# Performance work log

Hardware: AMD Instinct MI355X
Metric: run time of the kernel (lower is better)

Reference implementation:

```python
import jax, jax.numpy as jnp
from jax import lax
import numpy as np

EMBED, HIDDEN, VOCAB = 512, 512, 10000
ATT, ENC = 512, 2048
B, NPIX, T = 128, 49, 30


def _lin(k, out_d, in_d):
    k1, k2 = jax.random.split(k)
    s = 1.0 / np.sqrt(in_d)
    return (jax.random.uniform(k1, (out_d, in_d), minval=-s, maxval=s),
            jax.random.uniform(k2, (out_d,), minval=-s, maxval=s))


def setup_inputs() -> dict:
    key = jax.random.key(0)
    ks = jax.random.split(key, 24)
    inp = {}
    inp['enc_image'] = jax.random.normal(ks[0], (B, NPIX, ENC))
    inp['global_features'] = jax.random.normal(ks[1], (B, ENC))
    inp['encoded_captions'] = jax.random.randint(ks[2], (B, T), 0, VOCAB)
    lens = jax.random.randint(ks[3], (B,), 1, T + 1).at[0].set(T)
    inp['caption_lengths'] = lens[:, None]
    # parameters
    inp['emb_W'] = jax.random.uniform(ks[4], (VOCAB, EMBED), minval=-0.1, maxval=0.1)
    inp['e2h_W'], inp['e2h_b'] = _lin(ks[5], HIDDEN, ENC)
    inp['gf_W'], inp['gf_b'] = _lin(ks[6], EMBED, ENC)
    inp['fc_W'] = jax.random.uniform(ks[7], (VOCAB, HIDDEN), minval=-0.1, maxval=0.1)
    inp['fc_b'] = jnp.zeros((VOCAB,))
    inp['lstm_Wih'], inp['lstm_bih'] = _lin(ks[8], 4 * HIDDEN, 2 * EMBED)
    inp['lstm_Whh'], inp['lstm_bhh'] = _lin(ks[9], 4 * HIDDEN, HIDDEN)
    inp['xg_W'], inp['xg_b'] = _lin(ks[10], HIDDEN, 2 * EMBED)
    inp['hg_W'], inp['hg_b'] = _lin(ks[11], HIDDEN, HIDDEN)
    inp['senaff_W'], inp['senaff_b'] = _lin(ks[12], HIDDEN, HIDDEN)
    inp['senatt_W'], inp['senatt_b'] = _lin(ks[13], ATT, HIDDEN)
    inp['haff_W'], inp['haff_b'] = _lin(ks[14], HIDDEN, HIDDEN)
    inp['hatt_W'], inp['hatt_b'] = _lin(ks[15], ATT, HIDDEN)
    inp['vatt_W'], inp['vatt_b'] = _lin(ks[16], ATT, HIDDEN)
    inp['alph_W'], inp['alph_b'] = _lin(ks[17], 1, ATT)
    inp['ctx_W'], inp['ctx_b'] = _lin(ks[18], HIDDEN, HIDDEN)
    return inp


def reference(enc_image, global_features, encoded_captions, caption_lengths,
              emb_W, e2h_W, e2h_b, gf_W, gf_b, fc_W, fc_b,
              lstm_Wih, lstm_bih, lstm_Whh, lstm_bhh,
              xg_W, xg_b, hg_W, hg_b,
              senaff_W, senaff_b, senatt_W, senatt_b,
              haff_W, haff_b, hatt_W, hatt_b,
              vatt_W, vatt_b, alph_W, alph_b, ctx_W, ctx_b):
    lengths = caption_lengths[:, 0]
    order = jnp.argsort(-lengths)                     # descending (stable)
    lengths = lengths[order]
    spatial = jax.nn.relu(jnp.einsum('bpe,he->bph', enc_image[order], e2h_W) + e2h_b)  # (B,NP,H)
    gimg = jax.nn.relu(global_features[order] @ gf_W.T + gf_b)                          # (B,E)
    embs = emb_W[encoded_captions[order]]                                               # (B,T,E)
    inputs = jnp.concatenate([embs, jnp.broadcast_to(gimg[:, None, :], embs.shape)], axis=-1)  # (B,T,2E)
    vattn = jnp.einsum('bph,ah->bpa', spatial, vatt_W) + vatt_b                         # (B,NP,A) hoisted
    h0 = jnp.zeros((spatial.shape[0], HIDDEN), spatial.dtype)
    c0 = h0

    def step(carry, xs):
        h, c = carry
        xt, mask = xs                                  # (B,2E), (B,) bool = row still active
        gates = xt @ lstm_Wih.T + lstm_bih + h @ lstm_Whh.T + lstm_bhh
        i, f, g, o = jnp.split(gates, 4, axis=-1)
        c_new = jax.nn.sigmoid(f) * c + jax.nn.sigmoid(i) * jnp.tanh(g)
        h_new = jax.nn.sigmoid(o) * jnp.tanh(c_new)
        st = jax.nn.sigmoid(xt @ xg_W.T + xg_b + h @ hg_W.T + hg_b) * jnp.tanh(c_new)  # sentinel
        sen_aff = jax.nn.relu(st @ senaff_W.T + senaff_b)    # (B,H)
        sen_att = sen_aff @ senatt_W.T + senatt_b            # (B,A)
        h_aff = jnp.tanh(h_new @ haff_W.T + haff_b)
        h_att = h_aff @ hatt_W.T + hatt_b
        att_feats = jnp.concatenate([vattn, sen_att[:, None, :]], axis=1)   # (B,NP+1,A)
        scores = jnp.tanh(att_feats + h_att[:, None, :]) @ alph_W[0] + alph_b[0]
        alpha = jax.nn.softmax(scores, axis=1)               # (B,NP+1)
        cat_feats = jnp.concatenate([spatial, sen_aff[:, None, :]], axis=1)
        context = jnp.einsum('bph,bp->bh', cat_feats, alpha)
        out_l = jnp.tanh((context + h_aff) @ ctx_W.T + ctx_b)
        pt = out_l @ fc_W.T + fc_b                           # dropout = identity (eval)
        m = mask[:, None]
        return (jnp.where(m, h_new, h), jnp.where(m, c_new, c)), jnp.where(m, pt, 0.0)

    masks = lengths[None, :] > jnp.arange(T)[:, None]        # (T,B) replicates shrinking batch_size_t
    _, preds = lax.scan(step, (h0, c0), (jnp.swapaxes(inputs, 0, 1), masks))
    return jnp.swapaxes(preds, 0, 1)                         # (B,T,VOCAB), sorted-by-length order
```

## Files before the change

kernel.cpp:

```cpp
#include <hip/hip_runtime.h>
#include <hip/hip_bf16.h>
#include <cstdint>
#include <cstddef>

#define DEVI __device__ __forceinline__

#define BB 128
#define TT 30
#define VOCAB 10000
#define ENCD 2048
#define NPIX 49
#define SLOT 65536

typedef __attribute__((ext_vector_type(8))) short bf16x8;
typedef __attribute__((ext_vector_type(4))) float f32x4;

DEVI float bf2f(unsigned short u){ union{float f; unsigned int i;} x; x.i=((unsigned)u)<<16; return x.f; }
DEVI unsigned short f2bf(float f){ union{float f; unsigned int i;} x; x.f=f; unsigned r=x.i + 0x7fffu + ((x.i>>16)&1u); return (unsigned short)(r>>16); }
DEVI float sigm(float x){ return 1.0f/(1.0f+expf(-x)); }
DEVI f32x4 mfma16(bf16x8 a, bf16x8 b, f32x4 c){ return __builtin_amdgcn_mfma_f32_16x16x32_bf16(a,b,c,0,0,0); }

DEVI void waitflags(int* flags, int thresh){
  __syncthreads();
  if(threadIdx.x < 64){
    for(;;){
      int v = (threadIdx.x<32) ? __hip_atomic_load(&flags[threadIdx.x], __ATOMIC_RELAXED, __HIP_MEMORY_SCOPE_AGENT)
                               : 0x7fffffff;
      if(__all(v >= thresh)) break;
      __builtin_amdgcn_s_sleep(1);
    }
    __builtin_amdgcn_fence(__ATOMIC_ACQUIRE, "agent");
  }
  __syncthreads();
}
DEVI void signal(int* flag, int val){
  __syncthreads();
  if(threadIdx.x==0) __hip_atomic_store(flag, val, __ATOMIC_RELEASE, __HIP_MEMORY_SCOPE_AGENT);
}

__global__ void k_sort(const int* __restrict__ lens, int* __restrict__ order, int* __restrict__ Bt){
  __shared__ int L[BB];
  int i = threadIdx.x;
  L[i] = lens[i];
  __syncthreads();
  int li = L[i]; int rank = 0;
  for(int j=0;j<BB;j++){ int lj=L[j]; rank += (lj>li) || (lj==li && j<i); }
  order[rank] = i;
  if(i<TT){ int c=0; for(int j=0;j<BB;j++) c += (L[j]>i); Bt[i]=c; }
}

struct WC13 { const float* src[13]; unsigned short* dst[13]; int n[13]; };
__global__ void k_wconv(WC13 wc){
  int stride = gridDim.x*blockDim.x;
  int tid0 = blockIdx.x*blockDim.x + threadIdx.x;
  for(int s=0;s<13;s++){
    const float4* src=(const float4*)wc.src[s];
    int n4 = wc.n[s]>>2;
    ushort4* dst=(ushort4*)wc.dst[s];
    for(int i=tid0;i<n4;i+=stride){
      float4 v=src[i];
      ushort4 o; o.x=f2bf(v.x); o.y=f2bf(v.y); o.z=f2bf(v.z); o.w=f2bf(v.w);
      dst[i]=o;
    }
  }
}

__global__ void k_xt(const int* __restrict__ caps, const int* __restrict__ order,
                     const float* __restrict__ embW, const unsigned short* __restrict__ gimg,
                     unsigned short* __restrict__ xt){
  int total=BB*TT*1024;
  for(int idx=blockIdx.x*blockDim.x+threadIdx.x; idx<total; idx+=gridDim.x*blockDim.x){
    int k=idx&1023; int bt=idx>>10; int t=bt%TT; int b=bt/TT;
    unsigned short v;
    if(k<512){ int tok=caps[order[b]*TT+t]; v=f2bf(embW[(size_t)tok*512+k]); }
    else v=gimg[b*512+(k-512)];
    xt[idx]=v;
  }
}

__global__ __launch_bounds__(256) void k_gemm_f32A2(
    const float* __restrict__ A, int lda, int rpb, const int* __restrict__ order,
    const unsigned short* __restrict__ W, const float* __restrict__ bias,
    unsigned short* __restrict__ out, int K)
{
  __shared__ unsigned short As[128][136];
  int tid=threadIdx.x, wave=tid>>6, lane=tid&63, l15=lane&15, l4=lane>>4;
  int mb = blockIdx.y*128;
  f32x4 acc[8][4];
  f32x4 z = {0.f,0.f,0.f,0.f};
  #pragma unroll
  for(int i=0;i<8;i++)
    #pragma unroll
    for(int j=0;j<4;j++) acc[i][j]=z;
  int cch=tid&15, r0=tid>>4;
  int nb = blockIdx.x*256 + wave*64;
  for(int kc=0;kc<K;kc+=128){
    __syncthreads();
    #pragma unroll
    for(int rp=0;rp<8;rp++){
      int r=r0+rp*16;
      int m=mb+r;
      int sb = order[m/rpb]*rpb + m%rpb;
      const float* p = A + (size_t)sb*lda + kc + cch*8;
      float4 v0=*(const float4*)p, v1=*(const float4*)(p+4);
      unsigned short* d=&As[r][cch*8];
      d[0]=f2bf(v0.x); d[1]=f2bf(v0.y); d[2]=f2bf(v0.z); d[3]=f2bf(v0.w);
      d[4]=f2bf(v1.x); d[5]=f2bf(v1.y); d[6]=f2bf(v1.z); d[7]=f2bf(v1.w);
    }
    __syncthreads();
    #pragma unroll
    for(int kk=0;kk<4;kk++){
      bf16x8 bfr[4];
      #pragma unroll
      for(int nt=0;nt<4;nt++)
        bfr[nt] = *(const bf16x8*)(W + (size_t)(nb+nt*16+l15)*K + kc + kk*32 + l4*8);
      #pragma unroll
      for(int mt=0;mt<8;mt++){
        bf16x8 af = *(const bf16x8*)&As[mt*16+l15][kk*32+l4*8];
        #pragma unroll
        for(int nt=0;nt<4;nt++) acc[mt][nt]=mfma16(af,bfr[nt],acc[mt][nt]);
      }
    }
  }
  #pragma unroll
  for(int nt=0;nt<4;nt++){
    int n = nb + nt*16 + l15;
    float bs = bias[n];
    #pragma unroll
    for(int mt=0;mt<8;mt++){
      #pragma unroll
      for(int j=0;j<4;j++){
        int row = mb + mt*16 + l4*4 + j;
        float v = acc[mt][nt][j]+bs; v = v>0.f ? v : 0.f;
        out[(size_t)row*512 + n] = f2bf(v);
      }
    }
  }
}

DEVI void dev_gemm512(unsigned short (*As)[136], const unsigned short* A, const unsigned short* W,
                      const float* bias, unsigned short* out, int act, int xtile, int mb){
  int tid=threadIdx.x, wave=tid>>6, lane=tid&63, l15=lane&15, l4=lane>>4;
  f32x4 acc[8];
  f32x4 z = {0.f,0.f,0.f,0.f};
  #pragma unroll
  for(int i=0;i<8;i++) acc[i]=z;
  int cch=tid&15, r0=tid>>4;
  int nrow = xtile*64 + wave*16 + l15;
  for(int kc=0;kc<512;kc+=128){
    __syncthreads();
    #pragma unroll
    for(int rp=0;rp<8;rp++){
      int r=r0+rp*16;
      *(uint4*)&As[r][cch*8] = *(const uint4*)(A + (size_t)(mb+r)*512 + kc + cch*8);
    }
    __syncthreads();
    #pragma unroll
    for(int kk=0;kk<4;kk++){
      bf16x8 bfr = *(const bf16x8*)(W + (size_t)nrow*512 + kc + kk*32 + l4*8);
      #pragma unroll
      for(int mt=0;mt<8;mt++){
        bf16x8 af = *(const bf16x8*)&As[mt*16+l15][kk*32+l4*8];
        acc[mt]=mfma16(af,bfr,acc[mt]);
      }
    }
  }
  float bs = bias ? bias[nrow] : 0.f;
  #pragma unroll
  for(int mt=0;mt<8;mt++){
    #pragma unroll
    for(int j=0;j<4;j++){
      int row = mb + mt*16 + l4*4 + j;
      float v = acc[mt][j]+bs;
      if(act==1) v = fmaxf(v,0.f);
      else if(act==2) v = tanhf(v);
      out[(size_t)row*512+nrow]=f2bf(v);
    }
  }
  __syncthreads();
}

struct PreD { const unsigned short* A; const unsigned short* W; const float* bias; unsigned short* out; };
struct PreD2 { PreD d[2]; };
__global__ __launch_bounds__(256) void k_pre(PreD2 dd){
  __shared__ unsigned short As[128][136];
  PreD g = dd.d[blockIdx.z];
  dev_gemm512(As, g.A, g.W, g.bias, g.out, 0, blockIdx.x, blockIdx.y*128);
}

struct PCtx {
  const unsigned short *xt, *w_ih, *w_hh, *w_xg, *w_hg;
  const unsigned short *w_saff, *w_satt, *w_haff, *w_hatt, *w_ctx, *w_fc;
  const unsigned short *vattn, *SC;
  const float *bih,*bhh,*bxg,*bhg, *sab,*stbias,*hab,*htb, *alW,*alb, *cxb, *fcb;
  const int *Bt;
  unsigned short *h_hist;
  unsigned short *stb;
  unsigned short *tbuf;
  float *dout;
  int *Lflag;
  int *Tflag;
};

DEVI void dev_lstm(unsigned short (*As)[136], const PCtx& p, int t, int jblk,
                   const unsigned short* hprev, unsigned short* hout, float creg[2][4]){
  int tid=threadIdx.x, wave=tid>>6, lane=tid&63, l15=lane&15, l4=lane>>4;
  int jb = jblk*16;
  f32x4 acc[2][5];
  f32x4 z = {0.f,0.f,0.f,0.f};
  #pragma unroll
  for(int m=0;m<2;m++)
    #pragma unroll
    for(int s=0;s<5;s++) acc[m][s]=z;
  int cch=tid&15, r0=tid>>4;
  for(int kc=0;kc<1536;kc+=128){
    __syncthreads();
    #pragma unroll
    for(int rp=0;rp<8;rp++){
      int r=r0+rp*16;
      int kg = kc + cch*8;
      const unsigned short* src;
      if(kg<1024) src = p.xt + (size_t)r*(TT*1024) + t*1024 + kg;
      else        src = hprev + (size_t)r*512 + (kg-1024);
      *(uint4*)&As[r][cch*8] = *(const uint4*)src;
    }
    __syncthreads();
    #pragma unroll
    for(int kk=0;kk<4;kk++){
      int kg = kc + kk*32 + l4*8;
      bf16x8 bfr[5];
      #pragma unroll
      for(int s=0;s<5;s++){
        int row = (s<4) ? (s*512 + jb + l15) : (jb + l15);
        const unsigned short* wp;
        if(s<4) wp = (kg<1024) ? (p.w_ih + (size_t)row*1024 + kg) : (p.w_hh + (size_t)row*512 + (kg-1024));
        else    wp = (kg<1024) ? (p.w_xg + (size_t)row*1024 + kg) : (p.w_hg + (size_t)row*512 + (kg-1024));
        bfr[s] = *(const bf16x8*)wp;
      }
      #pragma unroll
      for(int m=0;m<2;m++){
        int mt = wave*2+m;
        bf16x8 af = *(const bf16x8*)&As[mt*16+l15][kk*32+l4*8];
        #pragma unroll
        for(int s=0;s<5;s++) acc[m][s]=mfma16(af,bfr[s],acc[m][s]);
      }
    }
  }
  int bt = p.Bt[t];
  int j = jb + l15;
  float bi  = p.bih[j]      + p.bhh[j];
  float bff = p.bih[512+j]  + p.bhh[512+j];
  float bg  = p.bih[1024+j] + p.bhh[1024+j];
  float bo  = p.bih[1536+j] + p.bhh[1536+j];
  float bs  = p.bxg[j] + p.bhg[j];
  unsigned short* stt = p.stb + (size_t)t*SLOT;
  #pragma unroll
  for(int m=0;m<2;m++){
    int mt = wave*2+m;
    #pragma unroll
    for(int jj=0;jj<4;jj++){
      int b = mt*16 + l4*4 + jj;
      float iv = sigm(acc[m][0][jj]+bi);
      float fv = sigm(acc[m][1][jj]+bff);
      float gv = tanhf(acc[m][2][jj]+bg);
      float ov = sigm(acc[m][3][jj]+bo);
      float sv = sigm(acc[m][4][jj]+bs);
      float cn = fv*creg[m][jj] + iv*gv;
      float tc = tanhf(cn);
      size_t idx=(size_t)b*512+j;
      if(b<bt){ hout[idx]=f2bf(ov*tc); creg[m][jj]=cn; }
      else    { hout[idx]=hprev[idx]; }
      stt[idx]=f2bf(sv*tc);
    }
  }
}

DEVI void dev_attn(float* sS, float* sA, int b, const PCtx& p,
                   const unsigned short* satt, const unsigned short* hatt,
                   const unsigned short* scs, const unsigned short* sch,
                   unsigned short* outl){
  int tid=threadIdx.x; int gid=tid>>4, gl=tid&15;
  const unsigned short* ha = hatt + (size_t)b*512;
  #pragma unroll
  for(int rp=0;rp<4;rp++){
    int pp = rp*16 + gid;
    float s = 0.f;
    if(pp<50){
      const unsigned short* vp = (pp<NPIX) ? (p.vattn + ((size_t)b*NPIX + pp)*512)
                                           : (satt + (size_t)b*512);
      for(int k=gl*32;k<gl*32+32;k++) s += tanhf(bf2f(vp[k]) + bf2f(ha[k])) * p.alW[k];
    }
    #pragma unroll
    for(int off=8;off>=1;off>>=1) s += __shfl_xor(s, off);
    if(gl==0 && pp<50) sS[pp] = s + p.alb[0];
  }
  __syncthreads();
  if(tid==0){
    float m=-1e30f;
    for(int pp=0;pp<50;pp++) m = fmaxf(m, sS[pp]);
    float sum=0.f;
    for(int pp=0;pp<50;pp++){ float e=expf(sS[pp]-m); sA[pp]=e; sum+=e; }
    float inv=1.f/sum;
    for(int pp=0;pp<50;pp++) sA[pp]*=inv;
  }
  __syncthreads();
  float a49 = sA[49];
  for(int n=tid;n<512;n+=256){
    float acc = bf2f(sch[(size_t)b*512+n]) + a49*bf2f(scs[(size_t)b*512+n]) + p.cxb[n];
    const unsigned short* sp = p.SC + (size_t)b*NPIX*512 + n;
    for(int pp=0;pp<NPIX;pp++) acc += sA[pp]*bf2f(sp[(size_t)pp*512]);
    outl[(size_t)b*512+n] = f2bf(tanhf(acc));
  }
  __syncthreads();
}

DEVI void dev_fc(unsigned short (*As)[136], const PCtx& p, int t, int xtile,
                 const unsigned short* outl){
  int tid=threadIdx.x, wave=tid>>6, lane=tid&63, l15=lane&15, l4=lane>>4;
  int bt = p.Bt[t];
  f32x4 acc[8];
  f32x4 z = {0.f,0.f,0.f,0.f};
  #pragma unroll
  for(int i=0;i<8;i++) acc[i]=z;
  int cch=tid&15, r0=tid>>4;
  int nbase = xtile*64 + wave*16;
  int nr = nbase + l15; if(nr > VOCAB-1) nr = VOCAB-1;
  for(int kc=0;kc<512;kc+=128){
    __syncthreads();
    #pragma unroll
    for(int rp=0;rp<8;rp++){
      int r=r0+rp*16;
      *(uint4*)&As[r][cch*8] = *(const uint4*)(outl + (size_t)r*512 + kc + cch*8);
    }
    __syncthreads();
    #pragma unroll
    for(int kk=0;kk<4;kk++){
      bf16x8 bfr = *(const bf16x8*)(p.w_fc + (size_t)nr*512 + kc + kk*32 + l4*8);
      #pragma unroll
      for(int mt=0;mt<8;mt++){
        if(mt*16 < bt){
          bf16x8 af = *(const bf16x8*)&As[mt*16+l15][kk*32+l4*8];
          acc[mt]=mfma16(af,bfr,acc[mt]);
        }
      }
    }
  }
  int n = nbase + l15; bool nok = n < VOCAB;
  float bs = nok ? p.fcb[n] : 0.f;
  #pragma unroll
  for(int mt=0;mt<8;mt++){
    #pragma unroll
    for(int j=0;j<4;j++){
      int b = mt*16 + l4*4 + j;
      float v = (b<bt) ? (acc[mt][j]+bs) : 0.f;
      if(nok) p.dout[(size_t)b*(TT*VOCAB) + (size_t)t*VOCAB + n] = v;
    }
  }
  __syncthreads();
}

__global__ __launch_bounds__(256) void k_persist(PCtx p){
  __shared__ unsigned short As[128][136];
  __shared__ float sS[52];
  __shared__ float sA[52];
  int cb = blockIdx.x;
  if(cb < 32){
    float creg[2][4];
    #pragma unroll
    for(int m=0;m<2;m++)
      #pragma unroll
      for(int j=0;j<4;j++) creg[m][j]=0.f;
    for(int t=0;t<TT;t++){
      if(t>0) waitflags(p.Lflag, t);
      dev_lstm(As, p, t, cb, p.h_hist + (size_t)t*SLOT, p.h_hist + (size_t)(t+1)*SLOT, creg);
      signal(&p.Lflag[cb], t+1);
    }
  } else {
    int team = (cb-32)>>5, w = (cb-32)&31;
    unsigned short* S = p.tbuf + (size_t)team*7*SLOT;
    unsigned short *Saff=S, *Haff=S+SLOT, *Outl=S+2*SLOT, *Satt=S+3*SLOT,
                   *Hatt=S+4*SLOT, *Scs=S+5*SLOT, *Sch=S+6*SLOT;
    int* tf = p.Tflag + team*32;
    int it=0;
    for(int t=team; t<TT; t+=7, it++){
      waitflags(p.Lflag, t+1);
      if(w<8)       dev_gemm512(As, p.stb + (size_t)t*SLOT,        p.w_saff, p.sab, Saff, 1, w,   0);
      else if(w<16) dev_gemm512(As, p.h_hist + (size_t)(t+1)*SLOT, p.w_haff, p.hab, Haff, 2, w-8, 0);
      signal(&tf[w], it*3+1); waitflags(tf, it*3+1);
      if(w<8)       dev_gemm512(As, Saff, p.w_satt, p.stbias, Satt, 0, w,    0);
      else if(w<16) dev_gemm512(As, Haff, p.w_hatt, p.htb,    Hatt, 0, w-8,  0);
      else if(w<24) dev_gemm512(As, Saff, p.w_ctx,  nullptr,  Scs,  0, w-16, 0);
      else          dev_gemm512(As, Haff, p.w_ctx,  nullptr,  Sch,  0, w-24, 0);
      signal(&tf[w], it*3+2); waitflags(tf, it*3+2);
      for(int r=0;r<4;r++) dev_attn(sS, sA, w*4+r, p, Satt, Hatt, Scs, Sch, Outl);
      signal(&tf[w], it*3+3); waitflags(tf, it*3+3);
      for(int x=w; x<157; x+=32) dev_fc(As, p, t, x, Outl);
    }
  }
}

extern "C" void kernel_launch(void* const* d_in, const int* in_sizes, int n_in,
                              void* d_out, int out_size, void* d_ws, size_t ws_size,
                              hipStream_t stream)
{
  const float* enc  =(const float*)d_in[0];
  const float* gfeat=(const float*)d_in[1];
  const int*   caps =(const int*)d_in[2];
  const int*   lens =(const int*)d_in[3];
  const float* embW =(const float*)d_in[4];
  const float* e2hW =(const float*)d_in[5];  const float* e2hb=(const float*)d_in[6];
  const float* gfW  =(const float*)d_in[7];  const float* gfb =(const float*)d_in[8];
  const float* fcW  =(const float*)d_in[9];  const float* fcb =(const float*)d_in[10];
  const float* WihF =(const float*)d_in[11]; const float* bih =(const float*)d_in[12];
  const float* WhhF =(const float*)d_in[13]; const float* bhh =(const float*)d_in[14];
  const float* xgWF =(const float*)d_in[15]; const float* bxg =(const float*)d_in[16];
  const float* hgWF =(const float*)d_in[17]; const float* bhg =(const float*)d_in[18];
  const float* saWF =(const float*)d_in[19]; const float* sab =(const float*)d_in[20];
  const float* stWF =(const float*)d_in[21]; const float* stbias=(const float*)d_in[22];
  const float* haWF =(const float*)d_in[23]; const float* hab =(const float*)d_in[24];
  const float* htWF =(const float*)d_in[25]; const float* htb =(const float*)d_in[26];
  const float* vaWF =(const float*)d_in[27]; const float* vab =(const float*)d_in[28];
  const float* alW  =(const float*)d_in[29]; const float* alb =(const float*)d_in[30];
  const float* cxWF =(const float*)d_in[31]; const float* cxb =(const float*)d_in[32];

  char* base=(char*)d_ws; size_t off=0;
  auto alloc=[&](size_t bytes)->void*{ void* r=base+off; off += (bytes+255)&~(size_t)255; return r; };

  int* order=(int*)alloc(BB*4);
  int* Bt   =(int*)alloc(32*4);
  unsigned short* w_e2h =(unsigned short*)alloc((size_t)512*2048*2);
  unsigned short* w_gf  =(unsigned short*)alloc((size_t)512*2048*2);
  unsigned short* w_fc  =(unsigned short*)alloc((size_t)VOCAB*512*2);
  unsigned short* w_ih  =(unsigned short*)alloc((size_t)2048*1024*2);
  unsigned short* w_hh  =(unsigned short*)alloc((size_t)2048*512*2);
  unsigned short* w_xg  =(unsigned short*)alloc((size_t)512*1024*2);
  unsigned short* w_hg  =(unsigned short*)alloc((size_t)512*512*2);
  unsigned short* w_saff=(unsigned short*)alloc((size_t)512*512*2);
  unsigned short* w_satt=(unsigned short*)alloc((size_t)512*512*2);
  unsigned short* w_haff=(unsigned short*)alloc((size_t)512*512*2);
  unsigned short* w_hatt=(unsigned short*)alloc((size_t)512*512*2);
  unsigned short* w_vatt=(unsigned short*)alloc((size_t)512*512*2);
  unsigned short* w_ctx =(unsigned short*)alloc((size_t)512*512*2);
  unsigned short* spatial=(unsigned short*)alloc((size_t)BB*NPIX*512*2);
  unsigned short* vattn  =(unsigned short*)alloc((size_t)BB*NPIX*512*2);
  unsigned short* SC     =(unsigned short*)alloc((size_t)BB*NPIX*512*2);
  unsigned short* gimg   =(unsigned short*)alloc((size_t)BB*512*2);
  unsigned short* xt     =(unsigned short*)alloc((size_t)BB*TT*1024*2);
  int* flags =(int*)alloc(4096);
  unsigned short* tbuf=(unsigned short*)alloc((size_t)7*7*SLOT*2);

  unsigned short* stb_hist = w_e2h;
  unsigned short* h_hist   = spatial;

  k_sort<<<1,BB,0,stream>>>(lens, order, Bt);

  WC13 wc;
  const float* srcs[13] = {e2hW,gfW,fcW,WihF,WhhF,xgWF,hgWF,saWF,stWF,haWF,htWF,vaWF,cxWF};
  unsigned short* dsts[13] = {w_e2h,w_gf,w_fc,w_ih,w_hh,w_xg,w_hg,w_saff,w_satt,w_haff,w_hatt,w_vatt,w_ctx};
  int ns[13] = {512*2048,512*2048,VOCAB*512,2048*1024,2048*512,512*1024,512*512,512*512,512*512,512*512,512*512,512*512,512*512};
  for(int i=0;i<13;i++){ wc.src[i]=srcs[i]; wc.dst[i]=dsts[i]; wc.n[i]=ns[i]; }
  k_wconv<<<1024,256,0,stream>>>(wc);

  k_gemm_f32A2<<<dim3(2,NPIX),256,0,stream>>>(enc, ENCD, NPIX, order, w_e2h, e2hb, spatial, ENCD);
  k_gemm_f32A2<<<dim3(2,1),  256,0,stream>>>(gfeat, ENCD, 1, order, w_gf, gfb, gimg, ENCD);
  k_xt<<<1024,256,0,stream>>>(caps, order, embW, gimg, xt);
  {
    PreD2 dv{};
    dv.d[0] = PreD{spatial, w_vatt, vab,     vattn};
    dv.d[1] = PreD{spatial, w_ctx,  nullptr, SC};
    k_pre<<<dim3(8,NPIX,2),256,0,stream>>>(dv);
  }

  hipMemsetAsync(h_hist, 0, (size_t)SLOT*2, stream);
  hipMemsetAsync(flags, 0, 4096, stream);

  PCtx pc;
  pc.xt=xt; pc.w_ih=w_ih; pc.w_hh=w_hh; pc.w_xg=w_xg; pc.w_hg=w_hg;
  pc.w_saff=w_saff; pc.w_satt=w_satt; pc.w_haff=w_haff; pc.w_hatt=w_hatt; pc.w_ctx=w_ctx; pc.w_fc=w_fc;
  pc.vattn=vattn; pc.SC=SC;
  pc.bih=bih; pc.bhh=bhh; pc.bxg=bxg; pc.bhg=bhg;
  pc.sab=sab; pc.stbias=stbias; pc.hab=hab; pc.htb=htb;
  pc.alW=alW; pc.alb=alb; pc.cxb=cxb; pc.fcb=fcb;
  pc.Bt=Bt;
  pc.h_hist=h_hist; pc.stb=stb_hist; pc.tbuf=tbuf;
  pc.dout=(float*)d_out;
  pc.Lflag=flags; pc.Tflag=flags+64;

  k_persist<<<256,256,0,stream>>>(pc);
}
```

Measured before the change: 2.813 ms.

## Replace acquire fences with relaxed atomic loads for cross-block data, parallelize softmax

```diff
diff --git a/kernel.cpp b/kernel.cpp
--- a/kernel.cpp
+++ b/kernel.cpp
@@ -20,6 +20,16 @@
 DEVI float sigm(float x){ return 1.0f/(1.0f+expf(-x)); }
 DEVI f32x4 mfma16(bf16x8 a, bf16x8 b, f32x4 c){ return __builtin_amdgcn_mfma_f32_16x16x32_bf16(a,b,c,0,0,0); }
 
+DEVI uint4 byp16(const void* p){
+  const unsigned long long* q=(const unsigned long long*)p;
+  unsigned long long a=__hip_atomic_load(q,   __ATOMIC_RELAXED, __HIP_MEMORY_SCOPE_AGENT);
+  unsigned long long b=__hip_atomic_load(q+1, __ATOMIC_RELAXED, __HIP_MEMORY_SCOPE_AGENT);
+  uint4 r; r.x=(unsigned)a; r.y=(unsigned)(a>>32); r.z=(unsigned)b; r.w=(unsigned)(b>>32); return r;
+}
+DEVI unsigned byp4(const void* p){
+  return __hip_atomic_load((const unsigned*)p, __ATOMIC_RELAXED, __HIP_MEMORY_SCOPE_AGENT);
+}
+
 DEVI void waitflags(int* flags, int thresh){
   __syncthreads();
   if(threadIdx.x < 64){
@@ -29,8 +39,8 @@
       if(__all(v >= thresh)) break;
       __builtin_amdgcn_s_sleep(1);
     }
-    __builtin_amdgcn_fence(__ATOMIC_ACQUIRE, "agent");
-  }
+  }
+  asm volatile("" ::: "memory");
   __syncthreads();
 }
 DEVI void signal(int* flag, int val){
@@ -138,6 +148,7 @@
   }
 }
 
+template<int BYP>
 DEVI void dev_gemm512(unsigned short (*As)[136], const unsigned short* A, const unsigned short* W,
                       const float* bias, unsigned short* out, int act, int xtile, int mb){
   int tid=threadIdx.x, wave=tid>>6, lane=tid&63, l15=lane&15, l4=lane>>4;
@@ -152,7 +163,9 @@
     #pragma unroll
     for(int rp=0;rp<8;rp++){
       int r=r0+rp*16;
-      *(uint4*)&As[r][cch*8] = *(const uint4*)(A + (size_t)(mb+r)*512 + kc + cch*8);
+      const unsigned short* src = A + (size_t)(mb+r)*512 + kc + cch*8;
+      if(BYP) *(uint4*)&As[r][cch*8] = byp16(src);
+      else    *(uint4*)&As[r][cch*8] = *(const uint4*)src;
     }
     __syncthreads();
     #pragma unroll
@@ -185,7 +198,7 @@
 __global__ __launch_bounds__(256) void k_pre(PreD2 dd){
   __shared__ unsigned short As[128][136];
   PreD g = dd.d[blockIdx.z];
-  dev_gemm512(As, g.A, g.W, g.bias, g.out, 0, blockIdx.x, blockIdx.y*128);
+  dev_gemm512<0>(As, g.A, g.W, g.bias, g.out, 0, blockIdx.x, blockIdx.y*128);
 }
 
 struct PCtx {
@@ -219,10 +232,11 @@
     for(int rp=0;rp<8;rp++){
       int r=r0+rp*16;
       int kg = kc + cch*8;
-      const unsigned short* src;
-      if(kg<1024) src = p.xt + (size_t)r*(TT*1024) + t*1024 + kg;
-      else        src = hprev + (size_t)r*512 + (kg-1024);
-      *(uint4*)&As[r][cch*8] = *(const uint4*)src;
+      if(kg<1024){
+        *(uint4*)&As[r][cch*8] = *(const uint4*)(p.xt + (size_t)r*(TT*1024) + t*1024 + kg);
+      } else {
+        *(uint4*)&As[r][cch*8] = byp16(hprev + (size_t)r*512 + (kg-1024));
+      }
     }
     __syncthreads();
     #pragma unroll
@@ -269,7 +283,10 @@
       float tc = tanhf(cn);
       size_t idx=(size_t)b*512+j;
       if(b<bt){ hout[idx]=f2bf(ov*tc); creg[m][jj]=cn; }
-      else    { hout[idx]=hprev[idx]; }
+      else {
+        unsigned pr = byp4(hprev + (idx & ~(size_t)1));
+        hout[idx] = (j&1) ? (unsigned short)(pr>>16) : (unsigned short)pr;
+      }
       stt[idx]=f2bf(sv*tc);
     }
   }
@@ -286,30 +303,54 @@
     int pp = rp*16 + gid;
     float s = 0.f;
     if(pp<50){
-      const unsigned short* vp = (pp<NPIX) ? (p.vattn + ((size_t)b*NPIX + pp)*512)
-                                           : (satt + (size_t)b*512);
-      for(int k=gl*32;k<gl*32+32;k++) s += tanhf(bf2f(vp[k]) + bf2f(ha[k])) * p.alW[k];
+      const unsigned short* vp = p.vattn + ((size_t)b*NPIX + pp)*512;
+      const unsigned short* sa = satt + (size_t)b*512;
+      #pragma unroll 4
+      for(int kk=0;kk<16;kk++){
+        int k = gl*32 + kk*2;
+        unsigned hu = byp4(ha + k);
+        float h0=bf2f((unsigned short)hu), h1=bf2f((unsigned short)(hu>>16));
+        float a0,a1;
+        if(pp<NPIX){ a0=bf2f(vp[k]); a1=bf2f(vp[k+1]); }
+        else { unsigned su=byp4(sa + k); a0=bf2f((unsigned short)su); a1=bf2f((unsigned short)(su>>16)); }
+        s += tanhf(a0+h0)*p.alW[k] + tanhf(a1+h1)*p.alW[k+1];
+      }
     }
     #pragma unroll
     for(int off=8;off>=1;off>>=1) s += __shfl_xor(s, off);
     if(gl==0 && pp<50) sS[pp] = s + p.alb[0];
   }
   __syncthreads();
-  if(tid==0){
-    float m=-1e30f;
-    for(int pp=0;pp<50;pp++) m = fmaxf(m, sS[pp]);
-    float sum=0.f;
-    for(int pp=0;pp<50;pp++){ float e=expf(sS[pp]-m); sA[pp]=e; sum+=e; }
-    float inv=1.f/sum;
-    for(int pp=0;pp<50;pp++) sA[pp]*=inv;
+  if(tid<64){
+    float sv = (tid<50) ? sS[tid] : -1e30f;
+    float m = sv;
+    #pragma unroll
+    for(int off=32;off>=1;off>>=1) m = fmaxf(m, __shfl_xor(m, off));
+    float e = (tid<50) ? expf(sv-m) : 0.f;
+    float sum = e;
+    #pragma unroll
+    for(int off=32;off>=1;off>>=1) sum += __shfl_xor(sum, off);
+    if(tid<50) sA[tid] = e/sum;
   }
   __syncthreads();
   float a49 = sA[49];
-  for(int n=tid;n<512;n+=256){
-    float acc = bf2f(sch[(size_t)b*512+n]) + a49*bf2f(scs[(size_t)b*512+n]) + p.cxb[n];
-    const unsigned short* sp = p.SC + (size_t)b*NPIX*512 + n;
-    for(int pp=0;pp<NPIX;pp++) acc += sA[pp]*bf2f(sp[(size_t)pp*512]);
-    outl[(size_t)b*512+n] = f2bf(tanhf(acc));
+  {
+    int n0 = tid*2;
+    unsigned schU = byp4(sch + (size_t)b*512 + n0);
+    unsigned scsU = byp4(scs + (size_t)b*512 + n0);
+    float acc0 = bf2f((unsigned short)schU) + a49*bf2f((unsigned short)(schU>>16))*0.f;
+    float c0 = bf2f((unsigned short)schU), c1 = bf2f((unsigned short)(schU>>16));
+    float s0 = bf2f((unsigned short)scsU), s1 = bf2f((unsigned short)(scsU>>16));
+    acc0 = c0 + a49*s0 + p.cxb[n0];
+    float acc1 = c1 + a49*s1 + p.cxb[n0+1];
+    const unsigned short* sp = p.SC + (size_t)b*NPIX*512 + n0;
+    for(int pp=0;pp<NPIX;pp++){
+      unsigned u = *(const unsigned*)(sp + (size_t)pp*512);
+      acc0 += sA[pp]*bf2f((unsigned short)u);
+      acc1 += sA[pp]*bf2f((unsigned short)(u>>16));
+    }
+    unsigned o = ((unsigned)f2bf(tanhf(acc1))<<16) | (unsigned)f2bf(tanhf(acc0));
+    *(unsigned*)(outl + (size_t)b*512 + n0) = o;
   }
   __syncthreads();
 }
@@ -330,7 +371,7 @@
     #pragma unroll
     for(int rp=0;rp<8;rp++){
       int r=r0+rp*16;
-      *(uint4*)&As[r][cch*8] = *(const uint4*)(outl + (size_t)r*512 + kc + cch*8);
+      *(uint4*)&As[r][cch*8] = byp16(outl + (size_t)r*512 + kc + cch*8);
     }
     __syncthreads();
     #pragma unroll
@@ -384,13 +425,13 @@
     int it=0;
     for(int t=team; t<TT; t+=7, it++){
       waitflags(p.Lflag, t+1);
-      if(w<8)       dev_gemm512(As, p.stb + (size_t)t*SLOT,        p.w_saff, p.sab, Saff, 1, w,   0);
-      else if(w<16) dev_gemm512(As, p.h_hist + (size_t)(t+1)*SLOT, p.w_haff, p.hab, Haff, 2, w-8, 0);
+      if(w<8)       dev_gemm512<1>(As, p.stb + (size_t)t*SLOT,        p.w_saff, p.sab, Saff, 1, w,   0);
+      else if(w<16) dev_gemm512<1>(As, p.h_hist + (size_t)(t+1)*SLOT, p.w_haff, p.hab, Haff, 2, w-8, 0);
       signal(&tf[w], it*3+1); waitflags(tf, it*3+1);
-      if(w<8)       dev_gemm512(As, Saff, p.w_satt, p.stbias, Satt, 0, w,    0);
-      else if(w<16) dev_gemm512(As, Haff, p.w_hatt, p.htb,    Hatt, 0, w-8,  0);
-      else if(w<24) dev_gemm512(As, Saff, p.w_ctx,  nullptr,  Scs,  0, w-16, 0);
-      else          dev_gemm512(As, Haff, p.w_ctx,  nullptr,  Sch,  0, w-24, 0);
+      if(w<8)       dev_gemm512<1>(As, Saff, p.w_satt, p.stbias, Satt, 0, w,    0);
+      else if(w<16) dev_gemm512<1>(As, Haff, p.w_hatt, p.htb,    Hatt, 0, w-8,  0);
+      else if(w<24) dev_gemm512<1>(As, Saff, p.w_ctx,  nullptr,  Scs,  0, w-16, 0);
+      else          dev_gemm512<1>(As, Haff, p.w_ctx,  nullptr,  Sch,  0, w-24, 0);
       signal(&tf[w], it*3+2); waitflags(tf, it*3+2);
       for(int r=0;r<4;r++) dev_attn(sS, sA, w*4+r, p, Satt, Hatt, Scs, Sch, Outl);
       signal(&tf[w], it*3+3); waitflags(tf, it*3+3);
```

Result: faster. 2.403 ms (-14.6%).
